# Kernel tuning notes

Hardware: AMD Instinct MI355X
Metric: run time of the kernel (lower is better)

Reference implementation:

```python
import jax, jax.numpy as jnp
import numpy as np

GATE_SLOPE = 10.0
ALPHA = 0.8


def setup_inputs() -> dict:
    key = jax.random.key(0)
    k0, k1, k2, k3, k4, k5 = jax.random.split(key, 6)
    B, I, O, NB = 512, 128, 64, 8
    x = jax.random.normal(k0, (B, I), dtype=jnp.float32)
    k = jax.random.uniform(k1, (I, O, NB), dtype=jnp.float32) * 2.0 + 0.5
    Ec = jax.random.uniform(k2, (I, O, NB), dtype=jnp.float32) * 2.0 + 0.5
    Ps = jax.random.uniform(k3, (I, O, NB), dtype=jnp.float32) * 1.5 + 0.5
    bias = jax.random.normal(k4, (I, O, NB), dtype=jnp.float32) * 0.1
    coef = jax.random.normal(k5, (I, O, NB), dtype=jnp.float32)
    return {"x": x, "k": k, "Ec": Ec, "Ps": Ps, "bias": bias, "coef": coef}


def reference(x, k, Ec, Ps, bias, coef):
    # x: [B, I]; params: [I, O, NB]
    xe = x[:, :, None, None]  # [B, I, 1, 1], broadcasts against [I, O, NB]
    # The torch loop writes prev_x = x_sample each iteration, so sample b sees
    # x[b-1] as prev (x[-1] = 0 from the initial buffer). branch_sign is never
    # written back, so branch_snap == 1 always. prev is detached in torch.
    prev = jnp.concatenate([jnp.zeros_like(xe[:1]), xe[:-1]], axis=0)
    prev = jax.lax.stop_gradient(prev)

    is_moving_up = jax.nn.sigmoid(GATE_SLOPE * (xe - prev))          # [B,I,1,1]
    crossed_pos = jax.nn.sigmoid(GATE_SLOPE * (xe - Ec))             # [B,I,O,NB]
    crossed_neg = jax.nn.sigmoid(GATE_SLOPE * (-xe - Ec))            # [B,I,O,NB]
    switch_up = is_moving_up * crossed_pos
    switch_lo = (1.0 - is_moving_up) * crossed_neg
    # target = su*1 + sl*(-1) + (1 - su - sl)*branch_snap, branch_snap = 1
    target = switch_up - switch_lo + (1.0 - switch_up - switch_lo)
    branch_momentum = ALPHA + (1.0 - ALPHA) * target                 # alpha*1 + (1-alpha)*target
    basis = Ps * jnp.tanh(k * (xe + Ec * branch_momentum)) + bias    # [B,I,O,NB]
    return jnp.einsum('bion,ion->bo', basis, coef)                   # sum over (I, NB)
```

## Files before the change

### kernel.cpp

```cpp
#include <hip/hip_runtime.h>


#define GATE_C 14.426950408889634f
#define TANH_C 2.8853900817779268f

constexpr int B = 512, I = 128, O = 64, NB = 8, BT = 32;

__global__ __launch_bounds__(256) void fe_main(
    const float* __restrict__ x, const float* __restrict__ k,
    const float* __restrict__ Ec, const float* __restrict__ Ps,
    const float* __restrict__ bias, const float* __restrict__ coef,
    float* __restrict__ out)
{
  __shared__ float4 p_lds[I * NB];
  __shared__ float2 xc_lds[BT][I + 1];
  __shared__ float red[4];

  const int tid = threadIdx.x;
  const int o  = blockIdx.y;
  const int b0 = blockIdx.x * BT;

  float pbase = 0.f;
  for (int e = tid; e < I * NB; e += 256) {
    const int i = e >> 3, n = e & 7;
    const int g = (i * O + o) * NB + n;
    const float ec = Ec[g], kk = k[g], ps = Ps[g], cf = coef[g], bs = bias[g];
    const float pc = ps * cf;
    p_lds[e] = make_float4(ec, ec * GATE_C, kk * TANH_C, pc);
    pbase += fmaf(bs, cf, pc);
  }

  for (int e = tid; e < BT * I; e += 256) {
    const int bl = e >> 7, i = e & 127;
    const int bg = b0 + bl;
    const float xv = x[bg * I + i];
    const float pv = (bg == 0) ? 0.f : x[(bg - 1) * I + i];
    const float c = -0.4f * __builtin_amdgcn_rcpf(
        1.f + __builtin_amdgcn_exp2f(GATE_C * (xv - pv)));
    xc_lds[bl][i] = make_float2(xv, c);
  }

  #pragma unroll
  for (int m = 1; m < 64; m <<= 1) pbase += __shfl_xor(pbase, m);
  if ((tid & 63) == 0) red[tid >> 6] = pbase;
  __syncthreads();

  const int bl = tid >> 3, n = tid & 7;
  const float4* __restrict__ prow = p_lds + n;
  const float2* __restrict__ xrow = &xc_lds[bl][0];

  float acc = 0.f;
  #pragma unroll 4
  for (int i = 0; i < I; ++i) {
    const float2 xc = xrow[i];
    const float4 p  = prow[i * 8];
    const float sg = __builtin_amdgcn_rcpf(
        1.f + __builtin_amdgcn_exp2f(fmaf(xc.x, GATE_C, p.y)));
    const float bm    = fmaf(xc.y, sg, 1.f);
    const float inner = fmaf(p.x, bm, xc.x);
    const float r = __builtin_amdgcn_rcpf(
        1.f + __builtin_amdgcn_exp2f(p.z * inner));
    acc = fmaf(p.w, r, acc);
  }

  acc += __shfl_xor(acc, 1);
  acc += __shfl_xor(acc, 2);
  acc += __shfl_xor(acc, 4);

  if (n == 0) {
    const float base = red[0] + red[1] + red[2] + red[3];
    out[(b0 + bl) * O + o] = fmaf(-2.f, acc, base);
  }
}

extern "C" void kernel_launch(void* const* d_in, const int* in_sizes, int n_in,
                              void* d_out, int out_size, void* d_ws, size_t ws_size,
                              hipStream_t stream) {
  const float* x    = (const float*)d_in[0];
  const float* k    = (const float*)d_in[1];
  const float* Ec   = (const float*)d_in[2];
  const float* Ps   = (const float*)d_in[3];
  const float* bias = (const float*)d_in[4];
  const float* coef = (const float*)d_in[5];
  float* out = (float*)d_out;

  dim3 grid(B / BT, O);
  fe_main<<<grid, 256, 0, stream>>>(x, k, Ec, Ps, bias, coef, out);
}
```

Before: 27.56 us.

## Replace exp/rcp transcendentals with packed Pade tanh and split I across waves

Swaps the exp2+rcp sigmoid/tanh evaluations for a rational Pade tanh approximation computed on float2 packed vectors, using a bit-trick reciprocal seed with Newton refinement. Each block now covers a smaller batch tile and spreads the I reduction across four waves, combining the partial sums through shared memory. Parameters are packed in pairs of I for packed math. The aim is to take work off the transcendental unit and raise parallelism and occupancy. The cost is approximation error from the clamped Pade form, which may not hold for large arguments, plus an extra reduction barrier and more redundant parameter loads since there are more blocks.

```diff
diff --git a/kernel.cpp b/kernel.cpp
--- a/kernel.cpp
+++ b/kernel.cpp
@@ -2,18 +2,36 @@
 
 
 #define GATE_C 14.426950408889634f
-#define TANH_C 2.8853900817779268f
 
-constexpr int B = 512, I = 128, O = 64, NB = 8, BT = 32;
+typedef float f32x2 __attribute__((ext_vector_type(2)));
+typedef float f32x4 __attribute__((ext_vector_type(4)));
+typedef int   i32x2 __attribute__((ext_vector_type(2)));
 
-__global__ __launch_bounds__(256) void fe_main(
+constexpr int B = 512, I = 128, O = 64, NB = 8, BT = 8, IP = I / 2;
+
+__device__ __forceinline__ f32x2 pk_seed(f32x2 d) {
+  i32x2 yi = (i32x2)(0x7EF127EA) - __builtin_bit_cast(i32x2, d);
+  return __builtin_bit_cast(f32x2, yi);
+}
+__device__ __forceinline__ f32x2 pk_newton(f32x2 y, f32x2 d) {
+  return y * __builtin_elementwise_fma(-d, y, (f32x2)(2.f));
+}
+__device__ __forceinline__ f32x2 pk_clamp1(f32x2 t) {
+  t.x = fminf(fmaxf(t.x, -1.f), 1.f);
+  t.y = fminf(fmaxf(t.y, -1.f), 1.f);
+  return t;
+}
+
+__global__ __launch_bounds__(256, 6) void fe_main(
     const float* __restrict__ x, const float* __restrict__ k,
     const float* __restrict__ Ec, const float* __restrict__ Ps,
     const float* __restrict__ bias, const float* __restrict__ coef,
     float* __restrict__ out)
 {
-  __shared__ float4 p_lds[I * NB];
-  __shared__ float2 xc_lds[BT][I + 1];
+  __shared__ f32x4 pA[IP][NB];
+  __shared__ f32x4 pB[IP][NB];
+  __shared__ f32x4 xcp[BT][IP + 1];
+  __shared__ float racc[4][BT];
   __shared__ float red[4];
 
   const int tid = threadIdx.x;
@@ -21,23 +39,29 @@
   const int b0 = blockIdx.x * BT;
 
   float pbase = 0.f;
-  for (int e = tid; e < I * NB; e += 256) {
-    const int i = e >> 3, n = e & 7;
-    const int g = (i * O + o) * NB + n;
-    const float ec = Ec[g], kk = k[g], ps = Ps[g], cf = coef[g], bs = bias[g];
-    const float pc = ps * cf;
-    p_lds[e] = make_float4(ec, ec * GATE_C, kk * TANH_C, pc);
-    pbase += fmaf(bs, cf, pc);
+  for (int e = tid; e < IP * NB; e += 256) {
+    const int ip = e >> 3, nn = e & 7;
+    const int g0 = ((2 * ip) * O + o) * NB + nn, g1 = g0 + O * NB;
+    const float E0 = Ec[g0], E1 = Ec[g1];
+    const float K0 = k[g0],  K1 = k[g1];
+    const float pc0 = Ps[g0] * coef[g0], pc1 = Ps[g1] * coef[g1];
+    pA[ip][nn] = (f32x4){E0, E1, -5.f * E0, -5.f * E1};
+    pB[ip][nn] = (f32x4){K0, K1, pc0, pc1};
+    pbase += fmaf(bias[g0], coef[g0], bias[g1] * coef[g1]);
   }
 
-  for (int e = tid; e < BT * I; e += 256) {
-    const int bl = e >> 7, i = e & 127;
+  const float2* __restrict__ x2p = (const float2*)x;
+  for (int e = tid; e < BT * IP; e += 256) {
+    const int bl = e >> 6, ip = e & 63;
     const int bg = b0 + bl;
-    const float xv = x[bg * I + i];
-    const float pv = (bg == 0) ? 0.f : x[(bg - 1) * I + i];
-    const float c = -0.4f * __builtin_amdgcn_rcpf(
-        1.f + __builtin_amdgcn_exp2f(GATE_C * (xv - pv)));
-    xc_lds[bl][i] = make_float2(xv, c);
+    const float2 xv = x2p[bg * IP + ip];
+    float2 pv = make_float2(0.f, 0.f);
+    if (bg != 0) pv = x2p[(bg - 1) * IP + ip];
+    const float ch0 = -0.2f * __builtin_amdgcn_rcpf(
+        1.f + __builtin_amdgcn_exp2f(GATE_C * (xv.x - pv.x)));
+    const float ch1 = -0.2f * __builtin_amdgcn_rcpf(
+        1.f + __builtin_amdgcn_exp2f(GATE_C * (xv.y - pv.y)));
+    xcp[bl][ip] = (f32x4){xv.x, xv.y, ch0, ch1};
   }
 
   #pragma unroll
@@ -45,31 +69,56 @@
   if ((tid & 63) == 0) red[tid >> 6] = pbase;
   __syncthreads();
 
-  const int bl = tid >> 3, n = tid & 7;
-  const float4* __restrict__ prow = p_lds + n;
-  const float2* __restrict__ xrow = &xc_lds[bl][0];
+  const int n  = tid & 7;
+  const int bl = (tid >> 3) & 7;
+  const int iq = tid >> 6;
+  const f32x4* __restrict__ pArow = &pA[iq * 16][n];
+  const f32x4* __restrict__ pBrow = &pB[iq * 16][n];
+  const f32x4* __restrict__ xrow  = &xcp[bl][iq * 16];
 
-  float acc = 0.f;
-  #pragma unroll 4
-  for (int i = 0; i < I; ++i) {
-    const float2 xc = xrow[i];
-    const float4 p  = prow[i * 8];
-    const float sg = __builtin_amdgcn_rcpf(
-        1.f + __builtin_amdgcn_exp2f(fmaf(xc.x, GATE_C, p.y)));
-    const float bm    = fmaf(xc.y, sg, 1.f);
-    const float inner = fmaf(p.x, bm, xc.x);
-    const float r = __builtin_amdgcn_rcpf(
-        1.f + __builtin_amdgcn_exp2f(p.z * inner));
-    acc = fmaf(p.w, r, acc);
+  f32x2 acc = (f32x2)(0.f);
+  #pragma unroll
+  for (int it = 0; it < 16; ++it) {
+    const f32x4 xc = xrow[it];
+    const f32x4 a  = pArow[it * 8];
+    const f32x4 bb = pBrow[it * 8];
+    const f32x2 x2 = xc.lo, ch2 = xc.hi;
+    const f32x2 ec2 = a.lo, eg2 = a.hi;
+    const f32x2 kv2 = bb.lo, pc2 = bb.hi;
+
+    const f32x2 wg = __builtin_elementwise_fma(x2, (f32x2)(-5.f), eg2);
+    const f32x2 g2 = wg * wg;
+    const f32x2 gnum = __builtin_elementwise_fma(g2 + 105.f, g2, (f32x2)(945.f));
+    const f32x2 gden = __builtin_elementwise_fma(
+        __builtin_elementwise_fma(g2, (f32x2)(15.f), (f32x2)(420.f)), g2, (f32x2)(945.f));
+    const f32x2 rg = pk_newton(pk_seed(gden), gden);
+    const f32x2 tg = pk_clamp1(wg * gnum * rg);
+
+    const f32x2 bm = __builtin_elementwise_fma(ch2, tg + 1.f, (f32x2)(1.f));
+    const f32x2 inner = __builtin_elementwise_fma(ec2, bm, x2);
+    const f32x2 v  = kv2 * inner;
+    const f32x2 v2 = v * v;
+    const f32x2 tnum = __builtin_elementwise_fma(v2 + 105.f, v2, (f32x2)(945.f));
+    const f32x2 tden = __builtin_elementwise_fma(
+        __builtin_elementwise_fma(v2, (f32x2)(15.f), (f32x2)(420.f)), v2, (f32x2)(945.f));
+    f32x2 rt = pk_newton(pk_seed(tden), tden);
+    rt = pk_newton(rt, tden);
+    const f32x2 t = pk_clamp1(v * tnum * rt);
+
+    acc = __builtin_elementwise_fma(pc2, t, acc);
   }
 
-  acc += __shfl_xor(acc, 1);
-  acc += __shfl_xor(acc, 2);
-  acc += __shfl_xor(acc, 4);
+  float s = acc.x + acc.y;
+  s += __shfl_xor(s, 1);
+  s += __shfl_xor(s, 2);
+  s += __shfl_xor(s, 4);
+  if (n == 0) racc[iq][bl] = s;
+  __syncthreads();
 
-  if (n == 0) {
+  if (tid < BT) {
+    const float r = racc[0][tid] + racc[1][tid] + racc[2][tid] + racc[3][tid];
     const float base = red[0] + red[1] + red[2] + red[3];
-    out[(b0 + bl) * O + o] = fmaf(-2.f, acc, base);
+    out[(b0 + tid) * O + o] = r + base;
   }
 }
 
```

After: 31.48 us. +14.2%, slower.

## Split into prep kernel plus register-resident parameter main kernel

Applied to the files above, without the earlier changes.

Adds a prep kernel that precomputes transposed per-output parameter records, bias sums and per-sample gate terms into the workspace. The main kernel then keeps four parameter records per thread in registers, tiles over 8 samples instead of 32, and reduces across I through LDS and shuffles. This drops the strided gather and LDS staging of parameters from every block, but costs an extra launch and a workspace round trip. The old kernel is kept as a fallback for when the workspace is too small.

```diff
diff --git a/kernel.cpp b/kernel.cpp
--- a/kernel.cpp
+++ b/kernel.cpp
@@ -4,69 +4,149 @@
 #define GATE_C 14.426950408889634f
 #define TANH_C 2.8853900817779268f
 
-constexpr int B = 512, I = 128, O = 64, NB = 8, BT = 32;
+constexpr int B = 512, I = 128, O = 64, NB = 8, BT = 8;
+constexpr size_t PK_OFF  = 0;
+constexpr size_t PB_OFF  = (size_t)O * I * NB * 16;
+constexpr size_t XCH_OFF = PB_OFF + (size_t)O * I * NB * 4;
+constexpr size_t WS_NEED = XCH_OFF + (size_t)B * I * 8;
 
-__global__ __launch_bounds__(256) void fe_main(
+__device__ __forceinline__ float sig_neg(float u) {
+  return __builtin_amdgcn_rcpf(1.f + __builtin_amdgcn_exp2f(u));
+}
+
+__global__ __launch_bounds__(256) void fe_prep(
+    const float* __restrict__ x, const float* __restrict__ k,
+    const float* __restrict__ Ec, const float* __restrict__ Ps,
+    const float* __restrict__ bias, const float* __restrict__ coef,
+    float4* __restrict__ pk, float* __restrict__ pb, float2* __restrict__ xch)
+{
+  const int idx = blockIdx.x * 256 + threadIdx.x;
+  const int o = idx >> 10, i = (idx >> 3) & 127, n = idx & 7;
+  const int g = (i * O + o) * NB + n;
+  const float E = Ec[g], K = k[g], P = Ps[g], C = coef[g], Bs = bias[g];
+  const float pc = P * C;
+  pk[idx] = make_float4(E, E * GATE_C, K * TANH_C, pc);
+  pb[idx] = fmaf(Bs, C, pc);
+  const float xv = x[idx];
+  const float pv = (idx < I) ? 0.f : x[idx - I];
+  const float ch = -0.4f * sig_neg(GATE_C * (xv - pv));
+  xch[idx] = make_float2(xv, ch);
+}
+
+#define TERM(ACC, BL, S) {                                                  \
+    const float2 xc = xl[BL][i0 + 32 * (S)];                                \
+    const float sg = sig_neg(fmaf(xc.x, GATE_C, pr##S.y));                  \
+    const float bm = fmaf(xc.y, sg, 1.f);                                   \
+    const float inner = fmaf(pr##S.x, bm, xc.x);                            \
+    const float r = sig_neg(pr##S.z * inner);                               \
+    ACC = fmaf(pr##S.w, r, ACC); }
+
+#define ROW(ACC, BL) TERM(ACC, BL, 0) TERM(ACC, BL, 1) \
+                     TERM(ACC, BL, 2) TERM(ACC, BL, 3)
+
+#define NRED(ACC, BL) { float t = ACC;                                      \
+    t += __shfl_xor(t, 1); t += __shfl_xor(t, 2); t += __shfl_xor(t, 4);    \
+    if (n == 0) racc[BL][i0] = t; }
+
+__global__ __launch_bounds__(256, 6) void fe_main(
+    const float4* __restrict__ pk, const float* __restrict__ pb,
+    const float2* __restrict__ xch, float* __restrict__ out)
+{
+  __shared__ float2 xl[BT][I];
+  __shared__ float racc[BT][33];
+  __shared__ float red[4];
+
+  const int tid = threadIdx.x;
+  const int o  = blockIdx.y;
+  const int b0 = blockIdx.x * BT;
+  const int i0 = tid >> 3, n = tid & 7;
+
+  const int pbase_idx = (o * I + i0) * NB + n;
+  const float4 pr0 = pk[pbase_idx];
+  const float4 pr1 = pk[pbase_idx + 32 * NB];
+  const float4 pr2 = pk[pbase_idx + 64 * NB];
+  const float4 pr3 = pk[pbase_idx + 96 * NB];
+  float pbase = pb[pbase_idx]            + pb[pbase_idx + 32 * NB]
+              + pb[pbase_idx + 64 * NB]  + pb[pbase_idx + 96 * NB];
+
+  for (int e = tid; e < BT * I; e += 256)
+    xl[e >> 7][e & 127] = xch[b0 * I + e];
+
+  #pragma unroll
+  for (int m = 1; m < 64; m <<= 1) pbase += __shfl_xor(pbase, m);
+  if ((tid & 63) == 0) red[tid >> 6] = pbase;
+  __syncthreads();
+
+  float a0 = 0.f, a1 = 0.f, a2 = 0.f, a3 = 0.f,
+        a4 = 0.f, a5 = 0.f, a6 = 0.f, a7 = 0.f;
+  ROW(a0, 0) ROW(a1, 1) ROW(a2, 2) ROW(a3, 3)
+  ROW(a4, 4) ROW(a5, 5) ROW(a6, 6) ROW(a7, 7)
+
+  NRED(a0, 0) NRED(a1, 1) NRED(a2, 2) NRED(a3, 3)
+  NRED(a4, 4) NRED(a5, 5) NRED(a6, 6) NRED(a7, 7)
+  __syncthreads();
+
+  const int bl = tid >> 5, q = tid & 31;
+  float v = racc[bl][q];
+  v += __shfl_xor(v, 1);
+  v += __shfl_xor(v, 2);
+  v += __shfl_xor(v, 4);
+  v += __shfl_xor(v, 8);
+  v += __shfl_xor(v, 16);
+  if (q == 0) {
+    const float base = red[0] + red[1] + red[2] + red[3];
+    out[(b0 + bl) * O + o] = fmaf(-2.f, v, base);
+  }
+}
+
+__global__ __launch_bounds__(256) void fe_fb(
     const float* __restrict__ x, const float* __restrict__ k,
     const float* __restrict__ Ec, const float* __restrict__ Ps,
     const float* __restrict__ bias, const float* __restrict__ coef,
     float* __restrict__ out)
 {
   __shared__ float4 p_lds[I * NB];
-  __shared__ float2 xc_lds[BT][I + 1];
+  __shared__ float2 xc_lds[32][I + 1];
   __shared__ float red[4];
-
-  const int tid = threadIdx.x;
-  const int o  = blockIdx.y;
-  const int b0 = blockIdx.x * BT;
-
+  const int tid = threadIdx.x, o = blockIdx.y, b0 = blockIdx.x * 32;
   float pbase = 0.f;
   for (int e = tid; e < I * NB; e += 256) {
-    const int i = e >> 3, n = e & 7;
-    const int g = (i * O + o) * NB + n;
-    const float ec = Ec[g], kk = k[g], ps = Ps[g], cf = coef[g], bs = bias[g];
-    const float pc = ps * cf;
-    p_lds[e] = make_float4(ec, ec * GATE_C, kk * TANH_C, pc);
-    pbase += fmaf(bs, cf, pc);
+    const int i = e >> 3, nn = e & 7;
+    const int g = (i * O + o) * NB + nn;
+    const float E = Ec[g], K = k[g], P = Ps[g], C = coef[g], Bs = bias[g];
+    const float pc = P * C;
+    p_lds[e] = make_float4(E, E * GATE_C, K * TANH_C, pc);
+    pbase += fmaf(Bs, C, pc);
   }
-
-  for (int e = tid; e < BT * I; e += 256) {
+  for (int e = tid; e < 32 * I; e += 256) {
     const int bl = e >> 7, i = e & 127;
     const int bg = b0 + bl;
     const float xv = x[bg * I + i];
     const float pv = (bg == 0) ? 0.f : x[(bg - 1) * I + i];
-    const float c = -0.4f * __builtin_amdgcn_rcpf(
-        1.f + __builtin_amdgcn_exp2f(GATE_C * (xv - pv)));
+    const float c = -0.4f * sig_neg(GATE_C * (xv - pv));
     xc_lds[bl][i] = make_float2(xv, c);
   }
-
   #pragma unroll
   for (int m = 1; m < 64; m <<= 1) pbase += __shfl_xor(pbase, m);
   if ((tid & 63) == 0) red[tid >> 6] = pbase;
   __syncthreads();
-
   const int bl = tid >> 3, n = tid & 7;
   const float4* __restrict__ prow = p_lds + n;
   const float2* __restrict__ xrow = &xc_lds[bl][0];
-
   float acc = 0.f;
   #pragma unroll 4
   for (int i = 0; i < I; ++i) {
     const float2 xc = xrow[i];
     const float4 p  = prow[i * 8];
-    const float sg = __builtin_amdgcn_rcpf(
-        1.f + __builtin_amdgcn_exp2f(fmaf(xc.x, GATE_C, p.y)));
-    const float bm    = fmaf(xc.y, sg, 1.f);
+    const float sg = sig_neg(fmaf(xc.x, GATE_C, p.y));
+    const float bm = fmaf(xc.y, sg, 1.f);
     const float inner = fmaf(p.x, bm, xc.x);
-    const float r = __builtin_amdgcn_rcpf(
-        1.f + __builtin_amdgcn_exp2f(p.z * inner));
+    const float r = sig_neg(p.z * inner);
     acc = fmaf(p.w, r, acc);
   }
-
   acc += __shfl_xor(acc, 1);
   acc += __shfl_xor(acc, 2);
   acc += __shfl_xor(acc, 4);
-
   if (n == 0) {
     const float base = red[0] + red[1] + red[2] + red[3];
     out[(b0 + bl) * O + o] = fmaf(-2.f, acc, base);
@@ -84,6 +164,16 @@
   const float* coef = (const float*)d_in[5];
   float* out = (float*)d_out;
 
-  dim3 grid(B / BT, O);
-  fe_main<<<grid, 256, 0, stream>>>(x, k, Ec, Ps, bias, coef, out);
+  if (ws_size >= WS_NEED) {
+    float4* pk  = (float4*)((char*)d_ws + PK_OFF);
+    float*  pb  = (float*) ((char*)d_ws + PB_OFF);
+    float2* xch = (float2*)((char*)d_ws + XCH_OFF);
+    fe_prep<<<dim3(O * I * NB / 256), 256, 0, stream>>>(x, k, Ec, Ps, bias, coef,
+                                                        pk, pb, xch);
+    dim3 grid(B / BT, O);
+    fe_main<<<grid, 256, 0, stream>>>(pk, pb, xch, out);
+  } else {
+    dim3 grid(B / 32, O);
+    fe_fb<<<grid, 256, 0, stream>>>(x, k, Ec, Ps, bias, coef, out);
+  }
 }
```

Result: slower. 30.29 us (+9.9%).
